# Kernel optimization log

Hardware: AMD Instinct MI355X
Metric: run time of the kernel (lower is better)

The kernel has to match this reference:

```python
import jax, jax.numpy as jnp
import numpy as np

KNN, D, CONV_NUM, LEVELS, POOL_RATIO = 4, 64, 6, 3, 8
QN, RFN, NS, H, W = 4, 32, 4, 64, 64
CN = LEVELS * CONV_NUM  # 18 = 3 embed levels x 6 correlation variants


def instance_norm(x, eps=1e-5):
    # InstanceNorm2d(affine=False): normalize each (sample, channel) over H,W (biased var)
    m = x.mean(axis=(-2, -1), keepdims=True)
    v = x.var(axis=(-2, -1), keepdims=True)
    return (x - m) * jax.lax.rsqrt(v + eps)


def conv2d(x, w, b):
    y = jax.lax.conv_general_dilated(x, w, (1, 1), 'SAME', dimension_numbers=('NCHW', 'OIHW', 'NCHW'))
    return y + b[None, :, None, None]


def conv1x1x1(x, w, b):
    # Conv3d kernel 1x1x1 == pure channel mixing; x: (qn,C,ns,h,w), w: (Cout,Cin)
    return jnp.einsum('qcshw,oc->qoshw', x, w) + b[None, :, None, None, None]


def head(x, w1, b1, w2, b2, w3, b3):
    x = jax.nn.relu(conv2d(x, w1, b1))
    x = jax.nn.relu(conv2d(x, w2, b2))
    return conv2d(x, w3, b3)


def setup_inputs():
    key = jax.random.key(0)
    ks = iter(jax.random.split(key, 64))
    def rn(shape, scale=0.05):
        return jax.random.normal(next(ks), shape, jnp.float32) * scale
    inp = {'corr': jax.random.normal(next(ks), (QN, RFN, NS, CN, H, W), jnp.float32)}
    inp['scale_conv_w1'] = rn((D, CN * KNN)); inp['scale_conv_b1'] = rn((D,))
    inp['scale_conv_w2'] = rn((D, D)); inp['scale_conv_b2'] = rn((D,))
    inp['score_conv_w1'] = rn((D, LEVELS * KNN)); inp['score_conv_b1'] = rn((D,))
    inp['score_conv_w2'] = rn((D, D)); inp['score_conv_b2'] = rn((D,))
    for name, cout in (('scale_pred', 1), ('offset_pred', 2), ('score_pred', 1)):
        inp[name + '_w1'] = rn((D, D, 3, 3)); inp[name + '_b1'] = rn((D,))
        inp[name + '_w2'] = rn((D, D, 3, 3)); inp[name + '_b2'] = rn((D,))
        inp[name + '_w3'] = rn((cout, D, 3, 3)); inp[name + '_b3'] = rn((cout,))
    return inp


def _maps(corr, scale_conv_w1, scale_conv_b1, scale_conv_w2, scale_conv_b2,
          score_conv_w1, score_conv_b1, score_conv_w2, score_conv_b2,
          scale_pred_w1, scale_pred_b1, scale_pred_w2, scale_pred_b2, scale_pred_w3, scale_pred_b3,
          offset_pred_w1, offset_pred_b1, offset_pred_w2, offset_pred_b2, offset_pred_w3, offset_pred_b3,
          score_pred_w1, score_pred_b1, score_pred_w2, score_pred_b2, score_pred_w3, score_pred_b3):
    qn, rfn, ns, cn, h, w = corr.shape
    corr_n = instance_norm(corr)                         # score_norm
    # per-(scale,position) matching score per reference -> knn refs
    ref_score = corr_n.mean(axis=3)                      # qn,rfn,ns,h,w
    rs = jnp.moveaxis(ref_score, 1, -1)                  # qn,ns,h,w,rfn
    _, top_idx = jax.lax.top_k(rs, KNN)                  # qn,ns,h,w,knn
    feat = jnp.transpose(corr_n, (0, 2, 4, 5, 1, 3))     # qn,ns,h,w,rfn,cn
    knn_feat = jnp.take_along_axis(feat, top_idx[..., None], axis=4)  # qn,ns,h,w,knn,cn
    x_scale = jnp.transpose(knn_feat.reshape(qn, ns, h, w, KNN * cn), (0, 4, 1, 2, 3))  # qn,72,ns,h,w
    lvl = corr_n.reshape(qn, rfn, ns, LEVELS, CONV_NUM, h, w).mean(axis=4)  # per-level score
    lvl = jnp.transpose(lvl, (0, 2, 4, 5, 1, 3))         # qn,ns,h,w,rfn,3
    knn_lvl = jnp.take_along_axis(lvl, top_idx[..., None], axis=4)
    x_score = jnp.transpose(knn_lvl.reshape(qn, ns, h, w, KNN * LEVELS), (0, 4, 1, 2, 3))  # qn,12,ns,h,w
    xs = conv1x1x1(jax.nn.relu(conv1x1x1(x_scale, scale_conv_w1, scale_conv_b1)), scale_conv_w2, scale_conv_b2).max(axis=2)
    xc = conv1x1x1(jax.nn.relu(conv1x1x1(x_score, score_conv_w1, score_conv_b1)), score_conv_w2, score_conv_b2).max(axis=2)
    scales = head(xs, scale_pred_w1, scale_pred_b1, scale_pred_w2, scale_pred_b2, scale_pred_w3, scale_pred_b3)
    offsets = head(xc, offset_pred_w1, offset_pred_b1, offset_pred_w2, offset_pred_b2, offset_pred_w3, offset_pred_b3)
    scores = head(xc, score_pred_w1, score_pred_b1, score_pred_w2, score_pred_b2, score_pred_w3, score_pred_b3)
    return scores, scales, offsets


def reference(corr, scale_conv_w1, scale_conv_b1, scale_conv_w2, scale_conv_b2,
              score_conv_w1, score_conv_b1, score_conv_w2, score_conv_b2,
              scale_pred_w1, scale_pred_b1, scale_pred_w2, scale_pred_b2, scale_pred_w3, scale_pred_b3,
              offset_pred_w1, offset_pred_b1, offset_pred_w2, offset_pred_b2, offset_pred_w3, offset_pred_b3,
              score_pred_w1, score_pred_b1, score_pred_w2, score_pred_b2, score_pred_w3, score_pred_b3):
    scores, scales, offsets = _maps(corr, scale_conv_w1, scale_conv_b1, scale_conv_w2, scale_conv_b2,
                                    score_conv_w1, score_conv_b1, score_conv_w2, score_conv_b2,
                                    scale_pred_w1, scale_pred_b1, scale_pred_w2, scale_pred_b2, scale_pred_w3, scale_pred_b3,
                                    offset_pred_w1, offset_pred_b1, offset_pred_w2, offset_pred_b2, offset_pred_w3, offset_pred_b3,
                                    score_pred_w1, score_pred_b1, score_pred_w2, score_pred_b2, score_pred_w3, score_pred_b3)
    # parse_detection: argmax + advanced-index gathers
    qn = scores.shape[0]; h, w = scores.shape[-2:]
    sid = jnp.argmax(scores.reshape(qn, -1), axis=1)
    sy, sx = sid // w, sid % w
    q = jnp.arange(qn)
    off = offsets[q, :, sy, sx]                          # qn,2
    pos = (jnp.stack([sx, sy], -1).astype(scores.dtype) + off + 0.5) * POOL_RATIO - 0.5
    scl = 2.0 ** scales[q, 0, sy, sx]
    return pos, scl, scores, scales, offsets
```

## Files before the change

kernel.cpp:

```cpp
#include <hip/hip_runtime.h>

#define HW 4096

__global__ __launch_bounds__(256) void k_statsrs(
    const float* __restrict__ corr, float2* __restrict__ ss,
    float* __restrict__ rs,
    const float* __restrict__ p0, const float* __restrict__ p1,
    const float* __restrict__ p2, const float* __restrict__ p3,
    const float* __restrict__ p4, const float* __restrict__ p5,
    float* __restrict__ wT, const float* __restrict__ w1s,
    const float* __restrict__ w2s, const float* __restrict__ w1c,
    const float* __restrict__ w2c, float* __restrict__ wm) {
  int t = threadIdx.x;
  if (blockIdx.x >= 512) {
    int b = blockIdx.x - 512;
    if (b < 96) {
      int arr = b >> 4;
      int chunk = b & 15;
      const float* src = (arr == 0) ? p0
                         : (arr == 1) ? p1
                         : (arr == 2) ? p2
                         : (arr == 3) ? p3
                         : (arr == 4) ? p4 : p5;
      float* dst = wT + arr * 36864;
#pragma unroll
      for (int i = 0; i < 9; i++) {
        int e = chunk * 2304 + i * 256 + t;
        int oc = e / 576;
        int rem = e - oc * 576;
        dst[rem * 64 + oc] = src[e];
      }
    } else {
      int i = (b - 96) * 256 + t;
      if (i < 4608) {
        int c = i >> 6, o = i & 63;
        wm[i] = w1s[o * 72 + c];
      } else if (i < 8704) {
        int j = i - 4608;
        int c = j >> 6, o = j & 63;
        wm[i] = w2s[o * 64 + c];
      } else if (i < 9472) {
        int j = i - 8704;
        int c = j >> 6, o = j & 63;
        wm[i] = w1c[o * 12 + c];
      } else if (i < 13568) {
        int j = i - 9472;
        int c = j >> 6, o = j & 63;
        wm[i] = w2c[o * 64 + c];
      }
    }
    return;
  }
  int g = blockIdx.x;
  const float4* p = (const float4*)(corr + (size_t)g * 18 * HW);

  float s[18], s2[18];
#pragma unroll
  for (int c = 0; c < 18; c++) { s[c] = 0.f; s2[c] = 0.f; }
#pragma unroll
  for (int c = 0; c < 18; c++) {
#pragma unroll
    for (int i = 0; i < 4; i++) {
      float4 v = p[(c << 10) + (i << 8) + t];
      s[c] += v.x + v.y + v.z + v.w;
      s2[c] += v.x * v.x + v.y * v.y + v.z * v.z + v.w * v.w;
    }
  }
#pragma unroll
  for (int c = 0; c < 18; c++) {
#pragma unroll
    for (int o = 1; o < 64; o <<= 1) {
      s[c] += __shfl_xor(s[c], o, 64);
      s2[c] += __shfl_xor(s2[c], o, 64);
    }
  }
  __shared__ float lds_s[4][18], lds_s2[4][18];
  __shared__ float lds_scl[18], lds_shf[18];
  int wid = t >> 6;
  int ln = t & 63;
  if (ln < 18) {
    float vs = 0.f, vs2 = 0.f;
#pragma unroll
    for (int c = 0; c < 18; c++) {
      vs = (ln == c) ? s[c] : vs;
      vs2 = (ln == c) ? s2[c] : vs2;
    }
    lds_s[wid][ln] = vs;
    lds_s2[wid][ln] = vs2;
  }
  __syncthreads();
  if (t < 18) {
    float S = lds_s[0][t] + lds_s[1][t] + lds_s[2][t] + lds_s[3][t];
    float S2 = lds_s2[0][t] + lds_s2[1][t] + lds_s2[2][t] + lds_s2[3][t];
    float m = S * (1.f / HW);
    float var = S2 * (1.f / HW) - m * m;
    float r = rsqrtf(var + 1e-5f);
    ss[g * 18 + t] = make_float2(r, -m * r);
    lds_scl[t] = r;
    lds_shf[t] = -m * r;
  }
  __syncthreads();

  float shsum = 0.f;
#pragma unroll
  for (int c = 0; c < 18; c++) shsum += lds_shf[c];
  const float inv = 1.f / 18.f;
#pragma unroll
  for (int i = 0; i < 4; i++) {
    float4 acc = make_float4(0.f, 0.f, 0.f, 0.f);
#pragma unroll
    for (int c = 0; c < 18; c++) {
      float4 v = p[(c << 10) + (i << 8) + t];
      float sc = lds_scl[c];
      acc.x = fmaf(v.x, sc, acc.x);
      acc.y = fmaf(v.y, sc, acc.y);
      acc.z = fmaf(v.z, sc, acc.z);
      acc.w = fmaf(v.w, sc, acc.w);
    }
    float4 o;
    o.x = (acc.x + shsum) * inv;
    o.y = (acc.y + shsum) * inv;
    o.z = (acc.z + shsum) * inv;
    o.w = (acc.w + shsum) * inv;
    ((float4*)(rs + (size_t)g * HW))[(i << 8) + t] = o;
  }
}

__global__ __launch_bounds__(256) void k_topk(const float* __restrict__ rs,
                                              int* __restrict__ topidx) {
  __shared__ float st[32 * 256];
  int b = blockIdx.x;
  int pxc = b & 15;
  int ns = (b >> 4) & 3;
  int q = b >> 6;
  int t = threadIdx.x;
  int pxb = pxc * 256;
#pragma unroll 8
  for (int r = 0; r < 32; r++)
    st[r * 256 + t] = rs[((q * 32 + r) * 4 + ns) * HW + pxb + t];
  __syncthreads();
  float v[32];
#pragma unroll
  for (int r = 0; r < 32; r++) v[r] = st[r * 256 + t];
  unsigned mask = 0;
  int sel[4];
#pragma unroll
  for (int k = 0; k < 4; k++) {
    float best = -3.4e38f;
    int bi = 0;
#pragma unroll
    for (int r = 0; r < 32; r++) {
      bool take = (!(mask & (1u << r))) && (v[r] > best);
      best = take ? v[r] : best;
      bi = take ? r : bi;
    }
    sel[k] = bi;
    mask |= (1u << bi);
  }
  ((int4*)topidx)[(q * 4 + ns) * HW + pxb + t] =
      make_int4(sel[0], sel[1], sel[2], sel[3]);
}

__global__ __launch_bounds__(512, 4) void k_mlp3(
    const float* __restrict__ corr, const float2* __restrict__ ss,
    const int* __restrict__ topidx, const float* __restrict__ wm,
    const float* __restrict__ b1s, const float* __restrict__ b2s,
    const float* __restrict__ b1c, const float* __restrict__ b2c,
    float* __restrict__ xs, float* __restrict__ xc) {
  __shared__ float lx[72 * 64];
  __shared__ float lh[64 * 64];
  __shared__ float lxsc[12 * 64];
  int blk = blockIdx.x;
  int q = blk >> 8, pxg = blk & 255;
  int t = threadIdx.x;
  int wi = t & 63;
  int oseg = t >> 6;
  int ns = (t >> 4) & 3;
  int pxi = t & 15;
  int px = pxg * 16 + pxi;
  int k = oseg >> 1;
  int ch0 = (oseg & 1) * 9;

  int4 ti = ((const int4*)topidx)[(q * 4 + ns) * HW + px];
  int rk = (k == 0) ? ti.x : (k == 1) ? ti.y : (k == 2) ? ti.z : ti.w;

  const float* cb = corr + ((size_t)((q * 32) * 4 + ns) * 18 + ch0) * HW + px;
  float v[9];
#pragma unroll
  for (int j = 0; j < 9; j++) v[j] = 0.f;
#pragma unroll 4
  for (int r = 0; r < 32; r++) {
    const float* pr = cb + (size_t)r * (72 * HW);
    float x[9];
#pragma unroll
    for (int j = 0; j < 9; j++) x[j] = pr[(size_t)j * HW];
    bool m = (r == rk);
#pragma unroll
    for (int j = 0; j < 9; j++) v[j] = m ? x[j] : v[j];
  }
  const float2* sb = ss + ((q * 32 + rk) * 4 + ns) * 18 + ch0;
  float2 sh[9];
#pragma unroll
  for (int j = 0; j < 9; j++) sh[j] = sb[j];
#pragma unroll
  for (int j = 0; j < 9; j++)
    lx[(k * 18 + ch0 + j) * 64 + wi] = fmaf(v[j], sh[j].x, sh[j].y);
  __syncthreads();

#pragma unroll
  for (int m = 0; m < 2; m++) {
    int idx = m * 512 + t;
    if (idx < 768) {
      int l = idx >> 6, w2 = idx & 63;
      float sm = 0.f;
#pragma unroll
      for (int j = 0; j < 6; j++) sm += lx[(l * 6 + j) * 64 + w2];
      lxsc[l * 64 + w2] = sm * (1.f / 6.f);
    }
  }

  float h[8];
  const float* bp1 = b1s + oseg * 8;
#pragma unroll
  for (int o = 0; o < 8; o++) h[o] = bp1[o];
#pragma unroll
  for (int c = 0; c < 72; c++) {
    float x = lx[c * 64 + wi];
    const float* wr = wm + c * 64 + oseg * 8;
#pragma unroll
    for (int o = 0; o < 8; o++) h[o] = fmaf(wr[o], x, h[o]);
  }
#pragma unroll
  for (int o = 0; o < 8; o++) lh[(oseg * 8 + o) * 64 + wi] = fmaxf(h[o], 0.f);
  __syncthreads();

  float a[8];
  const float* bp2 = b2s + oseg * 8;
#pragma unroll
  for (int o = 0; o < 8; o++) a[o] = bp2[o];
#pragma unroll
  for (int c = 0; c < 64; c++) {
    float x = lh[c * 64 + wi];
    const float* wr = wm + 4608 + c * 64 + oseg * 8;
#pragma unroll
    for (int o = 0; o < 8; o++) a[o] = fmaf(wr[o], x, a[o]);
  }
#pragma unroll
  for (int o = 0; o < 8; o++) lx[(oseg * 8 + o) * 64 + wi] = a[o];
  __syncthreads();

#pragma unroll
  for (int m = 0; m < 2; m++) {
    int idx = m * 512 + t;
    int oc = idx >> 4, ppx = idx & 15;
    float v2 = lx[oc * 64 + ppx];
    v2 = fmaxf(v2, lx[oc * 64 + 16 + ppx]);
    v2 = fmaxf(v2, lx[oc * 64 + 32 + ppx]);
    v2 = fmaxf(v2, lx[oc * 64 + 48 + ppx]);
    xs[(size_t)(q * 64 + oc) * HW + pxg * 16 + ppx] = v2;
  }
  const float* bc1 = b1c + oseg * 8;
#pragma unroll
  for (int o = 0; o < 8; o++) h[o] = bc1[o];
#pragma unroll
  for (int c = 0; c < 12; c++) {
    float x = lxsc[c * 64 + wi];
    const float* wr = wm + 8704 + c * 64 + oseg * 8;
#pragma unroll
    for (int o = 0; o < 8; o++) h[o] = fmaf(wr[o], x, h[o]);
  }
#pragma unroll
  for (int o = 0; o < 8; o++) lh[(oseg * 8 + o) * 64 + wi] = fmaxf(h[o], 0.f);
  __syncthreads();

  const float* bc2 = b2c + oseg * 8;
#pragma unroll
  for (int o = 0; o < 8; o++) a[o] = bc2[o];
#pragma unroll
  for (int c = 0; c < 64; c++) {
    float x = lh[c * 64 + wi];
    const float* wr = wm + 9472 + c * 64 + oseg * 8;
#pragma unroll
    for (int o = 0; o < 8; o++) a[o] = fmaf(wr[o], x, a[o]);
  }
#pragma unroll
  for (int o = 0; o < 8; o++) lx[(oseg * 8 + o) * 64 + wi] = a[o];
  __syncthreads();

#pragma unroll
  for (int m = 0; m < 2; m++) {
    int idx = m * 512 + t;
    int oc = idx >> 4, ppx = idx & 15;
    float v2 = lx[oc * 64 + ppx];
    v2 = fmaxf(v2, lx[oc * 64 + 16 + ppx]);
    v2 = fmaxf(v2, lx[oc * 64 + 32 + ppx]);
    v2 = fmaxf(v2, lx[oc * 64 + 48 + ppx]);
    xc[(size_t)(q * 64 + oc) * HW + pxg * 16 + ppx] = v2;
  }
}

template <bool RELU>
__global__ __launch_bounds__(256) void k_conv3h(
    const float* __restrict__ in0, const float* __restrict__ in1,
    const float* __restrict__ in2, const float* __restrict__ w0,
    const float* __restrict__ w1, const float* __restrict__ w2,
    const float* __restrict__ bb0, const float* __restrict__ bb1,
    const float* __restrict__ bb2, float* __restrict__ o0,
    float* __restrict__ o1, float* __restrict__ o2) {
  __shared__ float tile[16 * 10 * 72];
  int b = blockIdx.x;
  int hi = b >> 5;
  int og = hi / 3;
  int head = hi - og * 3;
  int q = (b >> 3) & 3;
  int rt = b & 7;
  const float* in = head == 0 ? in0 : head == 1 ? in1 : in2;
  const float* wT = head == 0 ? w0 : head == 1 ? w1 : w2;
  const float* bb = head == 0 ? bb0 : head == 1 ? bb1 : bb2;
  float* outp = head == 0 ? o0 : head == 1 ? o1 : o2;

  int t = threadIdx.x;
  int w = t & 63;
  int wr = t >> 6;
  int lane4 = t & 15;
  int rgrp = t >> 4;
  float acc[2][16];
#pragma unroll
  for (int pr = 0; pr < 2; pr++)
#pragma unroll
    for (int o = 0; o < 16; o++) acc[pr][o] = 0.f;
  const float* inq = in + (size_t)q * 64 * HW;

  for (int icc = 0; icc < 4; icc++) {
    __syncthreads();
    if (t < 160) { tile[t * 72 + 3] = 0.f; tile[t * 72 + 68] = 0.f; }
#pragma unroll
    for (int p = 0; p < 10; p++) {
      int idx = p * 16 + rgrp;
      int ch = idx / 10;
      int r = idx - ch * 10;
      int grow = rt * 8 + r - 1;
      float4 val = make_float4(0.f, 0.f, 0.f, 0.f);
      if (grow >= 0 && grow < 64)
        val = *(const float4*)(inq + (size_t)(icc * 16 + ch) * HW + grow * 64 +
                               lane4 * 4);
      *(float4*)(tile + idx * 72 + 4 + lane4 * 4) = val;
    }
    __syncthreads();
#pragma unroll 2
    for (int ic = 0; ic < 16; ic++) {
      float xv[4][3];
      const float* tb = tile + (ic * 10 + wr * 2) * 72 + w + 3;
#pragma unroll
      for (int rr = 0; rr < 4; rr++)
#pragma unroll
        for (int dc = 0; dc < 3; dc++) xv[rr][dc] = tb[rr * 72 + dc];
      const float* wb = wT + (size_t)(icc * 16 + ic) * 9 * 64 + og * 16;
#pragma unroll
      for (int dr = 0; dr < 3; dr++)
#pragma unroll
        for (int dc = 0; dc < 3; dc++) {
          const float* wv = wb + (dr * 3 + dc) * 64;
#pragma unroll
          for (int o = 0; o < 16; o++) {
            float wj = wv[o];
            acc[0][o] = fmaf(wj, xv[0 + dr][dc], acc[0][o]);
            acc[1][o] = fmaf(wj, xv[1 + dr][dc], acc[1][o]);
          }
        }
    }
  }
#pragma unroll
  for (int pr = 0; pr < 2; pr++) {
    int orow = rt * 8 + wr * 2 + pr;
#pragma unroll
    for (int o = 0; o < 16; o++) {
      float rz = acc[pr][o] + bb[og * 16 + o];
      if (RELU) rz = fmaxf(rz, 0.f);
      outp[((size_t)q * 64 + og * 16 + o) * HW + orow * 64 + w] = rz;
    }
  }
}

__global__ __launch_bounds__(256) void k_convSh(
    const float* __restrict__ in0, const float* __restrict__ in1,
    const float* __restrict__ in2, const float* __restrict__ wt0,
    const float* __restrict__ wt1, const float* __restrict__ wt2,
    const float* __restrict__ bb0, const float* __restrict__ bb1,
    const float* __restrict__ bb2, float* __restrict__ o0,
    float* __restrict__ o1, float* __restrict__ o2) {
  __shared__ float tile[64 * 3 * 66];
  __shared__ float red[4 * 2 * 64];
  int b = blockIdx.x;
  int head = b >> 8;
  int q = (b >> 6) & 3;
  int row = b & 63;
  const float* in = head == 0 ? in0 : head == 1 ? in1 : in2;
  const float* wt = head == 0 ? wt0 : head == 1 ? wt1 : wt2;
  const float* bb = head == 0 ? bb0 : head == 1 ? bb1 : bb2;
  float* outp = head == 0 ? o0 : head == 1 ? o1 : o2;
  int noc = (head == 1) ? 2 : 1;

  int t = threadIdx.x;
  int w = t & 63;
  int sub = t >> 6;
  if (t < 192) { tile[t * 66] = 0.f; tile[t * 66 + 65] = 0.f; }
  __syncthreads();
  const float* inq = in + (size_t)q * 64 * HW;
#pragma unroll
  for (int i = 0; i < 48; i++) {
    int idx = i * 4 + sub;
    int ic = idx / 3;
    int r = idx - ic * 3;
    int grow = row + r - 1;
    float val = 0.f;
    if (grow >= 0 && grow < 64) val = inq[(size_t)ic * HW + grow * 64 + w];
    tile[idx * 66 + 1 + w] = val;
  }
  __syncthreads();
  float acc0 = 0.f, acc1 = 0.f;
#pragma unroll 4
  for (int i = 0; i < 16; i++) {
    int ic = sub * 16 + i;
    float x[9];
#pragma unroll
    for (int dr = 0; dr < 3; dr++)
#pragma unroll
      for (int dc = 0; dc < 3; dc++)
        x[dr * 3 + dc] = tile[(ic * 3 + dr) * 66 + w + dc];
    const float* wb = wt + (size_t)ic * 9;
#pragma unroll
    for (int j = 0; j < 9; j++) acc0 += wb[j] * x[j];
    if (noc == 2) {
      const float* wb1 = wt + 576 + (size_t)ic * 9;
#pragma unroll
      for (int j = 0; j < 9; j++) acc1 += wb1[j] * x[j];
    }
  }
  red[(sub * 2 + 0) * 64 + w] = acc0;
  if (noc == 2) red[(sub * 2 + 1) * 64 + w] = acc1;
  __syncthreads();
  if (t < 128) {
    int o = t >> 6;
    if (o < noc) {
      float s = red[(0 * 2 + o) * 64 + w] + red[(1 * 2 + o) * 64 + w] +
                red[(2 * 2 + o) * 64 + w] + red[(3 * 2 + o) * 64 + w] + bb[o];
      outp[((size_t)q * noc + o) * HW + row * 64 + w] = s;
    }
  }
}

__global__ __launch_bounds__(256) void k_final(const float* __restrict__ scores,
                                               const float* __restrict__ scales,
                                               const float* __restrict__ offsets,
                                               float* __restrict__ pos,
                                               float* __restrict__ sclo) {
  int q = blockIdx.x, t = threadIdx.x;
  float best = -3.4e38f;
  int bi = 1 << 30;
  for (int i = t; i < HW; i += 256) {
    float v = scores[q * HW + i];
    if (v > best) { best = v; bi = i; }
  }
  __shared__ float bv[256];
  __shared__ int bix[256];
  bv[t] = best;
  bix[t] = bi;
  __syncthreads();
  for (int s = 128; s > 0; s >>= 1) {
    if (t < s) {
      if (bv[t + s] > bv[t] || (bv[t + s] == bv[t] && bix[t + s] < bix[t])) {
        bv[t] = bv[t + s];
        bix[t] = bix[t + s];
      }
    }
    __syncthreads();
  }
  if (t == 0) {
    int sid = bix[0];
    int sy = sid >> 6, sx = sid & 63;
    float o0 = offsets[(q * 2 + 0) * HW + sid];
    float o1 = offsets[(q * 2 + 1) * HW + sid];
    pos[q * 2 + 0] = ((float)sx + o0 + 0.5f) * 8.f - 0.5f;
    pos[q * 2 + 1] = ((float)sy + o1 + 0.5f) * 8.f - 0.5f;
    sclo[q] = exp2f(scales[q * HW + sid]);
  }
}

extern "C" void kernel_launch(void* const* d_in, const int* in_sizes, int n_in,
                              void* d_out, int out_size, void* d_ws, size_t ws_size,
                              hipStream_t stream) {
  const float* corr = (const float*)d_in[0];
  const float* w1s = (const float*)d_in[1];
  const float* b1s = (const float*)d_in[2];
  const float* w2s = (const float*)d_in[3];
  const float* b2s = (const float*)d_in[4];
  const float* w1c = (const float*)d_in[5];
  const float* b1c = (const float*)d_in[6];
  const float* w2c = (const float*)d_in[7];
  const float* b2c = (const float*)d_in[8];

  float* out = (float*)d_out;
  float* pos = out;
  float* sclo = out + 8;
  float* scores = out + 12;
  float* scales = out + 12 + 16384;
  float* offsets = out + 12 + 32768;

  char* ws = (char*)d_ws;
  float2* st_ss = (float2*)(ws + 0);
  int* topidx = (int*)(ws + 73728);
  float* rs = (float*)(ws + 1122304);
  float* wT = (float*)(ws + 19996672);
  float* wmT = (float*)(ws + 20881408);
  float* xs = (float*)(ws + 20971520);
  float* xc = (float*)(ws + 25165824);
  float* t1s = rs;
  float* t1o = (float*)((char*)rs + 4194304);
  float* t1c = (float*)((char*)rs + 8388608);
  float* t2c = (float*)((char*)rs + 12582912);
  float* t2s = xs;
  float* t2o = xc;

  k_statsrs<<<661, 256, 0, stream>>>(
      corr, st_ss, rs, (const float*)d_in[9], (const float*)d_in[11],
      (const float*)d_in[15], (const float*)d_in[17], (const float*)d_in[21],
      (const float*)d_in[23], wT, w1s, w2s, w1c, w2c, wmT);
  k_topk<<<256, 256, 0, stream>>>(rs, topidx);
  k_mlp3<<<1024, 512, 0, stream>>>(corr, st_ss, topidx, wmT, b1s, b2s, b1c,
                                   b2c, xs, xc);
  k_conv3h<true><<<384, 256, 0, stream>>>(
      xs, xc, xc, wT, wT + 2 * 36864, wT + 4 * 36864,
      (const float*)d_in[10], (const float*)d_in[16], (const float*)d_in[22],
      t1s, t1o, t1c);
  k_conv3h<true><<<384, 256, 0, stream>>>(
      t1s, t1o, t1c, wT + 1 * 36864, wT + 3 * 36864, wT + 5 * 36864,
      (const float*)d_in[12], (const float*)d_in[18], (const float*)d_in[24],
      t2s, t2o, t2c);
  k_convSh<<<768, 256, 0, stream>>>(
      t2s, t2o, t2c, (const float*)d_in[13], (const float*)d_in[19],
      (const float*)d_in[25], (const float*)d_in[14], (const float*)d_in[20],
      (const float*)d_in[26], scales, offsets, scores);

  k_final<<<4, 256, 0, stream>>>(scores, scales, offsets, pos, sclo);
}
```

Baseline: 622.1 us.

## Split top-k corr gather into separate kernel reading corr once

New measurement: 587.4 us. -5.6%, faster.

```diff
diff --git a/kernel.cpp b/kernel.cpp
--- a/kernel.cpp
+++ b/kernel.cpp
@@ -161,9 +161,52 @@
       make_int4(sel[0], sel[1], sel[2], sel[3]);
 }
 
-__global__ __launch_bounds__(512, 4) void k_mlp3(
-    const float* __restrict__ corr, const float2* __restrict__ ss,
-    const int* __restrict__ topidx, const float* __restrict__ wm,
+__global__ __launch_bounds__(256) void k_gather(const float* __restrict__ corr,
+                                                const float2* __restrict__ ss,
+                                                const int* __restrict__ topidx,
+                                                float* __restrict__ vbuf) {
+  __shared__ float ls[32], lsh[32];
+  int b = blockIdx.x;
+  int c = b % 18;
+  int rest = b / 18;
+  int ns = rest & 3;
+  int pxc = (rest >> 2) & 15;
+  int q = rest >> 6;
+  int t = threadIdx.x;
+  int px = pxc * 256 + t;
+
+  if (t < 32) {
+    float2 v2 = ss[q * 2304 + t * 72 + ns * 18 + c];
+    ls[t] = v2.x;
+    lsh[t] = v2.y;
+  }
+  int4 ti = ((const int4*)topidx)[(q * 4 + ns) * HW + px];
+  int rk0 = ti.x, rk1 = ti.y, rk2 = ti.z, rk3 = ti.w;
+  __syncthreads();
+
+  const float* base = corr + (size_t)(((q * 32) * 4 + ns) * 18 + c) * HW + px;
+  float v0 = 0.f, v1 = 0.f, v2 = 0.f, v3 = 0.f;
+#pragma unroll
+  for (int r = 0; r < 32; r++) {
+    float x = base[(size_t)r * 72 * HW];
+    v0 = (rk0 == r) ? x : v0;
+    v1 = (rk1 == r) ? x : v1;
+    v2 = (rk2 == r) ? x : v2;
+    v3 = (rk3 == r) ? x : v3;
+  }
+  v0 = v0 * ls[rk0] + lsh[rk0];
+  v1 = v1 * ls[rk1] + lsh[rk1];
+  v2 = v2 * ls[rk2] + lsh[rk2];
+  v3 = v3 * ls[rk3] + lsh[rk3];
+  size_t ob = (size_t)((q * 4 + ns) * 72 + c) * HW + px;
+  vbuf[ob] = v0;
+  vbuf[ob + 18 * HW] = v1;
+  vbuf[ob + 36 * HW] = v2;
+  vbuf[ob + 54 * HW] = v3;
+}
+
+__global__ __launch_bounds__(512, 4) void k_mlp4(
+    const float* __restrict__ vbuf, const float* __restrict__ wm,
     const float* __restrict__ b1s, const float* __restrict__ b2s,
     const float* __restrict__ b1c, const float* __restrict__ b2c,
     float* __restrict__ xs, float* __restrict__ xc) {
@@ -175,36 +218,17 @@
   int t = threadIdx.x;
   int wi = t & 63;
   int oseg = t >> 6;
-  int ns = (t >> 4) & 3;
-  int pxi = t & 15;
-  int px = pxg * 16 + pxi;
-  int k = oseg >> 1;
-  int ch0 = (oseg & 1) * 9;
-
-  int4 ti = ((const int4*)topidx)[(q * 4 + ns) * HW + px];
-  int rk = (k == 0) ? ti.x : (k == 1) ? ti.y : (k == 2) ? ti.z : ti.w;
-
-  const float* cb = corr + ((size_t)((q * 32) * 4 + ns) * 18 + ch0) * HW + px;
-  float v[9];
-#pragma unroll
-  for (int j = 0; j < 9; j++) v[j] = 0.f;
-#pragma unroll 4
-  for (int r = 0; r < 32; r++) {
-    const float* pr = cb + (size_t)r * (72 * HW);
-    float x[9];
-#pragma unroll
-    for (int j = 0; j < 9; j++) x[j] = pr[(size_t)j * HW];
-    bool m = (r == rk);
-#pragma unroll
-    for (int j = 0; j < 9; j++) v[j] = m ? x[j] : v[j];
-  }
-  const float2* sb = ss + ((q * 32 + rk) * 4 + ns) * 18 + ch0;
-  float2 sh[9];
-#pragma unroll
-  for (int j = 0; j < 9; j++) sh[j] = sb[j];
-#pragma unroll
-  for (int j = 0; j < 9; j++)
-    lx[(k * 18 + ch0 + j) * 64 + wi] = fmaf(v[j], sh[j].x, sh[j].y);
+  int px0 = pxg * 16;
+
+  const float* vq = vbuf + (size_t)(q * 4) * 72 * HW + px0;
+#pragma unroll
+  for (int j = 0; j < 9; j++) {
+    int e = j * 512 + t;
+    int c = e >> 6;
+    int w2 = e & 63;
+    int nns = w2 >> 4, ppx = w2 & 15;
+    lx[c * 64 + w2] = vq[(size_t)(nns * 72 + c) * HW + ppx];
+  }
   __syncthreads();
 
 #pragma unroll
@@ -257,7 +281,7 @@
     v2 = fmaxf(v2, lx[oc * 64 + 16 + ppx]);
     v2 = fmaxf(v2, lx[oc * 64 + 32 + ppx]);
     v2 = fmaxf(v2, lx[oc * 64 + 48 + ppx]);
-    xs[(size_t)(q * 64 + oc) * HW + pxg * 16 + ppx] = v2;
+    xs[(size_t)(q * 64 + oc) * HW + px0 + ppx] = v2;
   }
   const float* bc1 = b1c + oseg * 8;
 #pragma unroll
@@ -295,7 +319,7 @@
     v2 = fmaxf(v2, lx[oc * 64 + 16 + ppx]);
     v2 = fmaxf(v2, lx[oc * 64 + 32 + ppx]);
     v2 = fmaxf(v2, lx[oc * 64 + 48 + ppx]);
-    xc[(size_t)(q * 64 + oc) * HW + pxg * 16 + ppx] = v2;
+    xc[(size_t)(q * 64 + oc) * HW + px0 + ppx] = v2;
   }
 }
 
@@ -511,14 +535,15 @@
   float2* st_ss = (float2*)(ws + 0);
   int* topidx = (int*)(ws + 73728);
   float* rs = (float*)(ws + 1122304);
+  float* vbuf = rs;
   float* wT = (float*)(ws + 19996672);
   float* wmT = (float*)(ws + 20881408);
   float* xs = (float*)(ws + 20971520);
   float* xc = (float*)(ws + 25165824);
-  float* t1s = rs;
-  float* t1o = (float*)((char*)rs + 4194304);
-  float* t1c = (float*)((char*)rs + 8388608);
-  float* t2c = (float*)((char*)rs + 12582912);
+  float* t1s = vbuf;
+  float* t1o = (float*)((char*)vbuf + 4194304);
+  float* t1c = (float*)((char*)vbuf + 8388608);
+  float* t2c = (float*)((char*)vbuf + 12582912);
   float* t2s = xs;
   float* t2o = xc;
 
@@ -527,8 +552,8 @@
       (const float*)d_in[15], (const float*)d_in[17], (const float*)d_in[21],
       (const float*)d_in[23], wT, w1s, w2s, w1c, w2c, wmT);
   k_topk<<<256, 256, 0, stream>>>(rs, topidx);
-  k_mlp3<<<1024, 512, 0, stream>>>(corr, st_ss, topidx, wmT, b1s, b2s, b1c,
-                                   b2c, xs, xc);
+  k_gather<<<4608, 256, 0, stream>>>(corr, st_ss, topidx, vbuf);
+  k_mlp4<<<1024, 512, 0, stream>>>(vbuf, wmT, b1s, b2s, b1c, b2c, xs, xc);
   k_conv3h<true><<<384, 256, 0, stream>>>(
       xs, xc, xc, wT, wT + 2 * 36864, wT + 4 * 36864,
       (const float*)d_in[10], (const float*)d_in[16], (const float*)d_in[22],
```
